# Kernel optimization log

Hardware: AMD Instinct MI355X
Metric: run time of the kernel (lower is better)

## Reference

```python
import jax, jax.numpy as jnp
import numpy as np

B, C, H, W = 16, 96, 64, 64
N = H * W
BN = B * N
K = 16  # neighbors per node
E = BN * K
C_OUT = 96


def setup_inputs() -> dict:
    key = jax.random.key(0)
    k1, k2, k3, k4 = jax.random.split(key, 4)
    x = jax.random.normal(k1, (B, C, H, W), dtype=jnp.float32)
    # KNN-style edge list over flat node ids (node = b*N + n):
    # every node appears K times as a target (row 0), random sources (row 1).
    dst = jnp.repeat(jnp.arange(BN, dtype=jnp.int64), K)
    src = jax.random.randint(k2, (E,), 0, BN, dtype=jnp.int64)
    edge_index = jnp.stack([dst, src], axis=0)
    Wc = jax.random.normal(k3, (C_OUT, 2 * C), dtype=jnp.float32) * 0.05
    bc = jax.random.normal(k4, (C_OUT,), dtype=jnp.float32) * 0.05
    return {"x": x, "edge_index": edge_index, "Wc": Wc, "bc": bc}


def reference(x, edge_index, Wc, bc):
    b, c, h, w = x.shape
    n = h * w
    # Flatten to node features [B*N, C] with node id = b*N + n
    feats = x.reshape(b, c, n).transpose(0, 2, 1).reshape(b * n, c)
    # Max-relative aggregation: gather, subtract, scatter-max over targets
    diff = feats[edge_index[1]] - feats[edge_index[0]]        # [E, C]
    agg = jax.ops.segment_max(diff, edge_index[0], num_segments=b * n)  # [BN, C]
    x_j = agg.reshape(b, n, c).transpose(0, 2, 1)             # [B, C, N]
    x_n = x.reshape(b, c, n)                                   # [B, C, N]
    # Interleaved channel concat: (x_0, xj_0, x_1, xj_1, ...) -> [B, 2C, N]
    cat = jnp.stack([x_n, x_j], axis=2).reshape(b, 2 * c, n)
    # BasicConv: 1x1 conv (GEMM over channels) + bias + ReLU
    out = jnp.einsum('oc,bcn->bon', Wc, cat) + bc[None, :, None]
    out = jax.nn.relu(out)
    return out.reshape(b, -1, h, w)
```

## Files before the change

### kernel.cpp

```cpp
#include <hip/hip_runtime.h>

#define B_   16
#define C_   96
#define N_   4096
#define BN_  65536
#define K_   16
#define E_   (BN_ * K_)

typedef __attribute__((ext_vector_type(8))) short bf16x8;
typedef __attribute__((ext_vector_type(4))) float f32x4;

union FragU { uint32_t u[4]; bf16x8 v; };

__device__ __forceinline__ uint32_t pack2_bf16(float a, float b) {
    uint32_t ua = __builtin_bit_cast(uint32_t, a);
    uint32_t ub = __builtin_bit_cast(uint32_t, b);
    ua = (ua + 0x7fffu + ((ua >> 16) & 1u)) >> 16;
    ub = (ub + 0x7fffu + ((ub >> 16) & 1u)) >> 16;
    return (ua & 0xffffu) | (ub << 16);
}
__device__ __forceinline__ float lo16f(uint32_t u) {
    return __builtin_bit_cast(float, u << 16);
}
__device__ __forceinline__ float hi16f(uint32_t u) {
    return __builtin_bit_cast(float, u & 0xffff0000u);
}

__global__ __launch_bounds__(256) void transpose_pack_k(const float* __restrict__ x,
                                                        ushort* __restrict__ feats_bf,
                                                        const float* __restrict__ Wc,
                                                        ushort* __restrict__ Wp) {
    int blk = blockIdx.x;
    if (blk >= 3072) {
        int t = (blk - 3072) * 256 + threadIdx.x;
        if (t >= 36 * 64) return;
        int fid = t >> 6, l = t & 63;
        int ks = fid / 6, to = fid % 6;
        int o = to * 16 + (l & 15), g = l >> 4;
        uint32_t packed[4];
#pragma unroll
        for (int h = 0; h < 4; h++) {
            int e0 = 2 * h, e1 = 2 * h + 1;
            int k0 = ks * 32 + 4 * g + (e0 & 3) + 16 * (e0 >> 2);
            int k1 = ks * 32 + 4 * g + (e1 & 3) + 16 * (e1 >> 2);
            int ko0 = (k0 < 96) ? 2 * k0 : 2 * (k0 - 96) + 1;
            int ko1 = (k1 < 96) ? 2 * k1 : 2 * (k1 - 96) + 1;
            packed[h] = pack2_bf16(Wc[(size_t)o * 192 + ko0],
                                   Wc[(size_t)o * 192 + ko1]);
        }
        ((uint4*)Wp)[t] = make_uint4(packed[0], packed[1], packed[2], packed[3]);
        return;
    }
    __shared__ float tile[32][65];
    int b   = blk / 192;
    int rem = blk - b * 192;
    int c0  = (rem >> 6) * 32;
    int n0  = (rem & 63) * 64;
    const float* xp = x + (size_t)b * C_ * N_;
    for (int t = threadIdx.x; t < 32 * 64; t += 256) {
        int c = t >> 6, n = t & 63;
        tile[c][n] = xp[(size_t)(c0 + c) * N_ + n0 + n];
    }
    __syncthreads();
    ushort* fp = feats_bf + ((size_t)b * N_ + n0) * C_ + c0;
    for (int t = threadIdx.x; t < 64 * 16; t += 256) {
        int n = t >> 4, cq = t & 15;
        uint32_t p = pack2_bf16(tile[2 * cq][n], tile[2 * cq + 1][n]);
        *(uint32_t*)(fp + (size_t)n * C_ + 2 * cq) = p;
    }
}

__global__ __launch_bounds__(512) void gconv_k(const ushort* __restrict__ feats,
                                               const int* __restrict__ src,
                                               const ushort* __restrict__ Wp,
                                               const float* __restrict__ bc,
                                               float* __restrict__ out) {
    __shared__ ushort A_lds[128 * 200];
    int tid = threadIdx.x;
    int w = tid >> 6, l = tid & 63;
    int blk = blockIdx.x;
    int b = blk >> 5;
    int n0 = (blk & 31) << 7;

    const ushort* fb = feats + ((size_t)b * N_ + n0) * C_;
#pragma unroll
    for (int i = 0; i < 3; i++) {
        int tau = i * 512 + tid;
        int n = tau / 12;
        int p = tau - n * 12;
        uint4 u = *(const uint4*)(fb + (size_t)n * C_ + 8 * p);
        if (n & 1) { uint32_t t0 = u.x, t1 = u.y; u.x = u.z; u.y = u.w; u.z = t0; u.w = t1; }
        int slot = p ^ ((n >> 1) & 7);
        *(uint4*)&A_lds[n * 200 + slot * 8] = u;
    }

#pragma unroll
    for (int s = 0; s < 2; s++) {
        int ln = s * 64 + (tid >> 3);
        int r  = tid & 7;
        size_t i = (size_t)b * N_ + n0 + ln;
        const int* sp = src + i * K_;

        float m[12];
#pragma unroll
        for (int j = 0; j < 12; j++) m[j] = -3.0e38f;

#pragma unroll
        for (int q = 0; q < 4; q++) {
            int4 iv = ((const int4*)sp)[q];
            int ids[4] = {iv.x, iv.y, iv.z, iv.w};
#pragma unroll
            for (int kk = 0; kk < 4; kk++) {
                const uint2* row = (const uint2*)(feats + (size_t)ids[kk] * C_);
#pragma unroll
                for (int j = 0; j < 3; j++) {
                    uint2 v = row[r + 8 * j];
                    m[4 * j + 0] = fmaxf(m[4 * j + 0], lo16f(v.x));
                    m[4 * j + 1] = fmaxf(m[4 * j + 1], hi16f(v.x));
                    m[4 * j + 2] = fmaxf(m[4 * j + 2], lo16f(v.y));
                    m[4 * j + 3] = fmaxf(m[4 * j + 3], hi16f(v.y));
                }
            }
        }

        const uint2* own = (const uint2*)(feats + i * (size_t)C_);
#pragma unroll
        for (int j = 0; j < 3; j++) {
            uint2 o = own[r + 8 * j];
            uint2 p;
            p.x = pack2_bf16(m[4 * j + 0] - lo16f(o.x), m[4 * j + 1] - hi16f(o.x));
            p.y = pack2_bf16(m[4 * j + 2] - lo16f(o.y), m[4 * j + 3] - hi16f(o.y));
            int qa = r + 8 * j;
            int idx = ln * 200 + ((96 + 4 * qa) ^ ((ln & 15) << 2));
            *(uint2*)&A_lds[idx] = p;
        }
    }
    __syncthreads();

    float bcr[6];
#pragma unroll
    for (int to = 0; to < 6; to++) bcr[to] = bc[to * 16 + (l & 15)];

    f32x4 acc[6];
#pragma unroll
    for (int to = 0; to < 6; to++) acc[to] = (f32x4){0.f, 0.f, 0.f, 0.f};

    const uint4* wp4 = (const uint4*)Wp;
    int g = l >> 4;
    int msk = (l & 15) << 2;
    int abase = (w * 16 + (l & 15)) * 200;

#pragma unroll
    for (int ks = 0; ks < 6; ks++) {
        FragU bfrag[6];
#pragma unroll
        for (int to = 0; to < 6; to++) {
            uint4 u = wp4[(ks * 6 + to) * 64 + l];
            bfrag[to].u[0] = u.x; bfrag[to].u[1] = u.y;
            bfrag[to].u[2] = u.z; bfrag[to].u[3] = u.w;
        }
        int k1 = ks * 32 + 4 * g;
        uint2 lo = *(const uint2*)&A_lds[abase + (k1 ^ msk)];
        uint2 hi = *(const uint2*)&A_lds[abase + ((k1 + 16) ^ msk)];
        FragU afrag;
        afrag.u[0] = lo.x; afrag.u[1] = lo.y;
        afrag.u[2] = hi.x; afrag.u[3] = hi.y;
#pragma unroll
        for (int to = 0; to < 6; to++)
            acc[to] = __builtin_amdgcn_mfma_f32_16x16x32_bf16(
                afrag.v, bfrag[to].v, acc[to], 0, 0, 0);
    }

    int nl = n0 + w * 16 + ((l >> 4) << 2);
#pragma unroll
    for (int to = 0; to < 6; to++) {
        int o = to * 16 + (l & 15);
        float4 v;
        v.x = fmaxf(acc[to][0] + bcr[to], 0.0f);
        v.y = fmaxf(acc[to][1] + bcr[to], 0.0f);
        v.z = fmaxf(acc[to][2] + bcr[to], 0.0f);
        v.w = fmaxf(acc[to][3] + bcr[to], 0.0f);
        *(float4*)(out + ((size_t)b * C_ + o) * N_ + nl) = v;
    }
}

extern "C" void kernel_launch(void* const* d_in, const int* in_sizes, int n_in,
                              void* d_out, int out_size, void* d_ws, size_t ws_size,
                              hipStream_t stream) {
    const float* x   = (const float*)d_in[0];
    const int*   ei  = (const int*)d_in[1];
    const float* Wc  = (const float*)d_in[2];
    const float* bc  = (const float*)d_in[3];
    float* out = (float*)d_out;

    const int* src = ei + E_;

    ushort* feats_bf = (ushort*)d_ws;
    ushort* Wp       = (ushort*)((char*)d_ws + (size_t)BN_ * C_ * 2);

    transpose_pack_k<<<3081, 256, 0, stream>>>(x, feats_bf, Wc, Wp);

    gconv_k<<<B_ * (N_ / 128), 512, 0, stream>>>(feats_bf, src, Wp, bc, out);
}
```

Measured before the change: 53.05 us.

## Halve node tile per block and split output channels across waves

Each block now handles 64 nodes instead of 128, doubling the grid to 1024 blocks. The MFMA stage is split across 8 waves as 4 node groups by 2 output-channel halves. Each node's own features are read from LDS rather than re-fetched from global memory, which needs an extra barrier after the LDS fill. This roughly halves LDS per block and is meant to improve occupancy and parallelism for the gather-bound phase, at the cost of an added sync and more blocks.

```diff
diff --git a/kernel.cpp b/kernel.cpp
--- a/kernel.cpp
+++ b/kernel.cpp
@@ -75,28 +75,29 @@
                                                const ushort* __restrict__ Wp,
                                                const float* __restrict__ bc,
                                                float* __restrict__ out) {
-    __shared__ ushort A_lds[128 * 200];
+    __shared__ ushort A_lds[64 * 200];
     int tid = threadIdx.x;
-    int w = tid >> 6, l = tid & 63;
     int blk = blockIdx.x;
-    int b = blk >> 5;
-    int n0 = (blk & 31) << 7;
+    int b = blk >> 6;
+    int n0 = (blk & 63) << 6;
 
     const ushort* fb = feats + ((size_t)b * N_ + n0) * C_;
 #pragma unroll
-    for (int i = 0; i < 3; i++) {
+    for (int i = 0; i < 2; i++) {
         int tau = i * 512 + tid;
-        int n = tau / 12;
-        int p = tau - n * 12;
-        uint4 u = *(const uint4*)(fb + (size_t)n * C_ + 8 * p);
-        if (n & 1) { uint32_t t0 = u.x, t1 = u.y; u.x = u.z; u.y = u.w; u.z = t0; u.w = t1; }
-        int slot = p ^ ((n >> 1) & 7);
-        *(uint4*)&A_lds[n * 200 + slot * 8] = u;
-    }
-
-#pragma unroll
-    for (int s = 0; s < 2; s++) {
-        int ln = s * 64 + (tid >> 3);
+        if (tau < 768) {
+            int n = tau / 12;
+            int p = tau - n * 12;
+            uint4 u = *(const uint4*)(fb + (size_t)n * C_ + 8 * p);
+            if (n & 1) { uint32_t t0 = u.x, t1 = u.y; u.x = u.z; u.y = u.w; u.z = t0; u.w = t1; }
+            int slot = p ^ ((n >> 1) & 7);
+            *(uint4*)&A_lds[n * 200 + slot * 8] = u;
+        }
+    }
+    __syncthreads();
+
+    {
+        int ln = tid >> 3;
         int r  = tid & 7;
         size_t i = (size_t)b * N_ + n0 + ln;
         const int* sp = src + i * K_;
@@ -123,41 +124,43 @@
             }
         }
 
-        const uint2* own = (const uint2*)(feats + i * (size_t)C_);
+        int omsk = (ln & 15) << 2;
 #pragma unroll
         for (int j = 0; j < 3; j++) {
-            uint2 o = own[r + 8 * j];
+            int qa = r + 8 * j;
+            uint2 o = *(const uint2*)&A_lds[ln * 200 + ((4 * qa) ^ omsk)];
             uint2 p;
             p.x = pack2_bf16(m[4 * j + 0] - lo16f(o.x), m[4 * j + 1] - hi16f(o.x));
             p.y = pack2_bf16(m[4 * j + 2] - lo16f(o.y), m[4 * j + 3] - hi16f(o.y));
-            int qa = r + 8 * j;
-            int idx = ln * 200 + ((96 + 4 * qa) ^ ((ln & 15) << 2));
-            *(uint2*)&A_lds[idx] = p;
+            *(uint2*)&A_lds[ln * 200 + ((96 + 4 * qa) ^ omsk)] = p;
         }
     }
     __syncthreads();
 
-    float bcr[6];
-#pragma unroll
-    for (int to = 0; to < 6; to++) bcr[to] = bc[to * 16 + (l & 15)];
-
-    f32x4 acc[6];
-#pragma unroll
-    for (int to = 0; to < 6; to++) acc[to] = (f32x4){0.f, 0.f, 0.f, 0.f};
+    int w = tid >> 6, l = tid & 63;
+    int tm = w >> 1, th = w & 1;
+
+    float bcr[3];
+#pragma unroll
+    for (int j = 0; j < 3; j++) bcr[j] = bc[(th * 3 + j) * 16 + (l & 15)];
+
+    f32x4 acc[3];
+#pragma unroll
+    for (int j = 0; j < 3; j++) acc[j] = (f32x4){0.f, 0.f, 0.f, 0.f};
 
     const uint4* wp4 = (const uint4*)Wp;
     int g = l >> 4;
     int msk = (l & 15) << 2;
-    int abase = (w * 16 + (l & 15)) * 200;
+    int abase = (tm * 16 + (l & 15)) * 200;
 
 #pragma unroll
     for (int ks = 0; ks < 6; ks++) {
-        FragU bfrag[6];
-#pragma unroll
-        for (int to = 0; to < 6; to++) {
-            uint4 u = wp4[(ks * 6 + to) * 64 + l];
-            bfrag[to].u[0] = u.x; bfrag[to].u[1] = u.y;
-            bfrag[to].u[2] = u.z; bfrag[to].u[3] = u.w;
+        FragU bfrag[3];
+#pragma unroll
+        for (int j = 0; j < 3; j++) {
+            uint4 u = wp4[(ks * 6 + th * 3 + j) * 64 + l];
+            bfrag[j].u[0] = u.x; bfrag[j].u[1] = u.y;
+            bfrag[j].u[2] = u.z; bfrag[j].u[3] = u.w;
         }
         int k1 = ks * 32 + 4 * g;
         uint2 lo = *(const uint2*)&A_lds[abase + (k1 ^ msk)];
@@ -166,20 +169,20 @@
         afrag.u[0] = lo.x; afrag.u[1] = lo.y;
         afrag.u[2] = hi.x; afrag.u[3] = hi.y;
 #pragma unroll
-        for (int to = 0; to < 6; to++)
-            acc[to] = __builtin_amdgcn_mfma_f32_16x16x32_bf16(
-                afrag.v, bfrag[to].v, acc[to], 0, 0, 0);
-    }
-
-    int nl = n0 + w * 16 + ((l >> 4) << 2);
-#pragma unroll
-    for (int to = 0; to < 6; to++) {
-        int o = to * 16 + (l & 15);
+        for (int j = 0; j < 3; j++)
+            acc[j] = __builtin_amdgcn_mfma_f32_16x16x32_bf16(
+                afrag.v, bfrag[j].v, acc[j], 0, 0, 0);
+    }
+
+    int nl = n0 + tm * 16 + ((l >> 4) << 2);
+#pragma unroll
+    for (int j = 0; j < 3; j++) {
+        int o = (th * 3 + j) * 16 + (l & 15);
         float4 v;
-        v.x = fmaxf(acc[to][0] + bcr[to], 0.0f);
-        v.y = fmaxf(acc[to][1] + bcr[to], 0.0f);
-        v.z = fmaxf(acc[to][2] + bcr[to], 0.0f);
-        v.w = fmaxf(acc[to][3] + bcr[to], 0.0f);
+        v.x = fmaxf(acc[j][0] + bcr[j], 0.0f);
+        v.y = fmaxf(acc[j][1] + bcr[j], 0.0f);
+        v.z = fmaxf(acc[j][2] + bcr[j], 0.0f);
+        v.w = fmaxf(acc[j][3] + bcr[j], 0.0f);
         *(float4*)(out + ((size_t)b * C_ + o) * N_ + nl) = v;
     }
 }
@@ -200,5 +203,5 @@
 
     transpose_pack_k<<<3081, 256, 0, stream>>>(x, feats_bf, Wc, Wp);
 
-    gconv_k<<<B_ * (N_ / 128), 512, 0, stream>>>(feats_bf, src, Wp, bc, out);
-}
+    gconv_k<<<BN_ / 64, 512, 0, stream>>>(feats_bf, src, Wp, bc, out);
+}
```

Result: faster. 50.55 us (-4.7%).
